# Performance work log

Hardware: AMD Instinct MI355X
Metric: run time of the kernel (lower is better)

The kernel has to match this reference:

```python
import jax, jax.numpy as jnp
import numpy as np

C = 5.0          # tanh clamp constant (args.c, non-trainable)
B, N, R, D = 4, 16, 64, 256  # batch, block_num, block_len, word_dim
NEG = -1e9


def setup_inputs() -> dict:
    key = jax.random.key(0)
    ks = iter(jax.random.split(key, 80))

    def W(i, o):
        # xavier-like init (torch stores (out,in); we store (in,out) and use x @ W)
        return jax.random.normal(next(ks), (i, o), jnp.float32) * np.float32(np.sqrt(2.0 / (i + o)))

    def bvec(d):
        return jax.random.normal(next(ks), (d,), jnp.float32) * 0.01

    inp = {"x": jax.random.normal(next(ks), (B, N, R, D), jnp.float32)}
    for p in ("fw", "bw"):
        inp[f"fcW_{p}"] = W(D, D);  inp[f"fcb_{p}"] = bvec(D)
        inp[f"mW1_{p}"] = W(D, D);  inp[f"mW2_{p}"] = W(D, D);  inp[f"mb_{p}"] = bvec(D)
        inp[f"s2tW1_{p}"] = W(D, D); inp[f"s2tb1_{p}"] = bvec(D)
        inp[f"s2tW_{p}"] = W(D, D);  inp[f"s2tb_{p}"] = bvec(D)
        inp[f"gW1_{p}"] = W(D, D);  inp[f"gW2_{p}"] = W(D, D);  inp[f"gb_{p}"] = bvec(D)
        inp[f"fW1_{p}"] = W(3 * D, D); inp[f"fb1_{p}"] = bvec(D)
        inp[f"fW2_{p}"] = W(3 * D, D); inp[f"fb2_{p}"] = bvec(D)
    return inp


def _mSA(x, W1, W2, b, fw):
    # x: (..., L, d) -> (..., L, d). Additive per-feature attention with strict
    # triangular mask. fw: token i attends to j > i (last row zeroed);
    # bw: token i attends to j < i (first row zeroed). Matches the torch
    # -inf mask + narrow + zero-pad construction exactly.
    L = x.shape[-2]
    xi = (x @ W1)[..., :, None, :]                 # (..., L, 1, d)
    xj = (x @ W2)[..., None, :, :]                 # (..., 1, L, d)
    f = C * jnp.tanh((xi + xj + b) / C)            # (..., i, j, d)
    i = jnp.arange(L)[:, None]
    j = jnp.arange(L)[None, :]
    allowed = (j > i) if fw else (j < i)           # (L, L)
    scores = jnp.where(allowed[..., None], f, NEG)
    att = jax.nn.softmax(scores, axis=-2)          # softmax over j
    rowvalid = (jnp.arange(L) < L - 1) if fw else (jnp.arange(L) > 0)
    att = att * rowvalid[:, None, None].astype(x.dtype)
    return jnp.einsum('...ijd,...jd->...id', att, x)


def _s2t(x, W1, b1, Wo, bo):
    # source2token self-attention: (..., L, d) -> (..., d)
    f = jax.nn.relu(x @ W1 + b1)
    a = jax.nn.softmax(f @ Wo + bo, axis=-2)
    return jnp.sum(a * x, axis=-2)


def _mblosa(x, mW1, mW2, mb, s2tW1, s2tb1, s2tW, s2tb,
            gW1, gW2, gb, fW1, fb1, fW2, fb2, fw):
    Bb, n, r, d = x.shape
    h = _mSA(x, mW1, mW2, mb, fw)                  # (B, n, r, d) intra-block
    v = _s2t(h, s2tW1, s2tb1, s2tW, s2tb)          # (B, n, d)    block summary
    o = _mSA(v, mW1, mW2, mb, fw)                  # (B, n, d)    inter-block
    G = jax.nn.sigmoid(o @ gW1 + v @ gW2 + gb)
    e = G * o + (1.0 - G) * v                      # (B, n, d)
    # torch: cat of e[i] repeated r times, then narrow(1, 0, n)
    idx = jnp.arange(n) // r
    E = e[:, idx]                                  # (B, n, d)
    # torch: flatten blocks then narrow(1, 0, n) (faithful to source)
    xf = x.reshape(Bb, n * r, d)[:, :n]
    hf = h.reshape(Bb, n * r, d)[:, :n]
    cat = jnp.concatenate([xf, hf, E], axis=-1)    # (B, n, 3d)
    fusion = jax.nn.relu(cat @ fW1 + fb1)
    Gf = jax.nn.sigmoid(cat @ fW2 + fb2)
    return Gf * fusion + (1.0 - Gf) * xf           # (B, n, d)


def reference(x,
              fcW_fw, fcb_fw, mW1_fw, mW2_fw, mb_fw, s2tW1_fw, s2tb1_fw,
              s2tW_fw, s2tb_fw, gW1_fw, gW2_fw, gb_fw, fW1_fw, fb1_fw,
              fW2_fw, fb2_fw,
              fcW_bw, fcb_bw, mW1_bw, mW2_bw, mb_bw, s2tW1_bw, s2tb1_bw,
              s2tW_bw, s2tb_bw, gW1_bw, gW2_bw, gb_bw, fW1_bw, fb1_bw,
              fW2_bw, fb2_bw):
    in_fw = jax.nn.relu(x @ fcW_fw + fcb_fw)
    in_bw = jax.nn.relu(x @ fcW_bw + fcb_bw)
    u_fw = _mblosa(in_fw, mW1_fw, mW2_fw, mb_fw, s2tW1_fw, s2tb1_fw,
                   s2tW_fw, s2tb_fw, gW1_fw, gW2_fw, gb_fw,
                   fW1_fw, fb1_fw, fW2_fw, fb2_fw, True)
    u_bw = _mblosa(in_bw, mW1_bw, mW2_bw, mb_bw, s2tW1_bw, s2tb1_bw,
                   s2tW_bw, s2tb_bw, gW1_bw, gW2_bw, gb_bw,
                   fW1_bw, fb1_bw, fW2_bw, fb2_bw, False)
    return jnp.concatenate([u_fw, u_bw], axis=-1)  # (B, n, 2d)
```

## Files before the change

### kernel.cpp

```cpp
#include <hip/hip_runtime.h>
#include <hip/hip_cooperative_groups.h>
#include <hip/hip_bf16.h>

typedef __hip_bfloat16 BF16;
typedef __attribute__((ext_vector_type(8))) short short8;
typedef __attribute__((ext_vector_type(4))) short short4v;
typedef __attribute__((ext_vector_type(4))) float f32x4;

#define MFMA_B16(a,b,c) __builtin_amdgcn_mfma_f32_16x16x32_bf16((a),(b),(c),0,0,0)

#if __has_builtin(__builtin_amdgcn_exp2f)
#define EXP2F(x) __builtin_amdgcn_exp2f(x)
#else
#define EXP2F(x) __expf(0.6931471805599453f * (x))
#endif

__device__ __forceinline__ short f2bs(float f){ BF16 h = __float2bfloat16(f); return *(short*)&h; }
__device__ __forceinline__ float bs2f(short s){ BF16 h = *(BF16*)&s; return __bfloat162float(h); }

struct SrcPack { const float* s[10]; };
struct GDir { const void* A0; const void* Al; const short* Wh; const short* Wl;
              const float* bias; void* O0; };
struct MbloDir { const short* Ah; const short* W1h; const short* W2h;
                 const float* mb; short* Hh; int fw; };
struct PoolDir { const short* T1; const short* Wh; const float* bias;
                 const short* Hh; float* V; };
struct Gate2Dir { const float* V; const float* W1; const float* W2; const float* mb;
                  const float* gW1; const float* gW2; const float* gb;
                  float* E0; int fw; };
struct FuseDir { const short* INh; const short* Hh;
                 const float* E0; const float* fW1; const float* fb1;
                 const float* fW2; const float* fb2; };


__global__ __launch_bounds__(256) void prep_k(SrcPack p, const float* __restrict__ X,
                                              short* __restrict__ Oh,
                                              short* __restrict__ Ol,
                                              short* __restrict__ Xh,
                                              short* __restrict__ Xl)
{
    if (blockIdx.y >= 10) {
        int u = (blockIdx.y - 10) * 16 + blockIdx.x;
        size_t base = (size_t)u * 16384;
        #pragma unroll
        for (int i = 0; i < 16; i++) {
            size_t idx = base + (size_t)i * 1024 + threadIdx.x * 4;
            float4 f = *(const float4*)(X + idx);
            short4v vh, vl;
            float t0[4] = {f.x, f.y, f.z, f.w};
            #pragma unroll
            for (int j = 0; j < 4; j++) {
                vh[j] = f2bs(t0[j]);
                vl[j] = f2bs(t0[j] - bs2f(vh[j]));
            }
            *(short4v*)(Xh + idx) = vh;
            *(short4v*)(Xl + idx) = vl;
        }
        return;
    }
    __shared__ float s[64][65];
    const float* W = p.s[blockIdx.y];
    short* oh = Oh + (size_t)blockIdx.y * 65536;
    short* ol = Ol + (size_t)blockIdx.y * 65536;
    int tr = (blockIdx.x >> 2) * 64, tc = (blockIdx.x & 3) * 64;
    #pragma unroll
    for (int i = 0; i < 16; i++) {
        int e = threadIdx.x + i * 256;
        int r = e >> 6, c = e & 63;
        s[c][r] = W[(size_t)(tr + r) * 256 + tc + c];
    }
    __syncthreads();
    #pragma unroll
    for (int i = 0; i < 16; i++) {
        int e = threadIdx.x + i * 256;
        int c2 = e >> 6, r2 = e & 63;
        float v = s[c2][r2];
        short hi = f2bs(v);
        short lo = f2bs(v - bs2f(hi));
        size_t oi = (size_t)(tc + c2) * 256 + tr + r2;
        oh[oi] = hi;
        ol[oi] = lo;
    }
}

template<int AM, int OM, int RELU, int BS>
__device__ __forceinline__ void gemm_body(const void* __restrict__ A0,
    const void* __restrict__ Alo,
    const short* __restrict__ Wh, const short* __restrict__ Wl,
    const float* __restrict__ bias, void* __restrict__ O0,
    int row0, int col0)
{
    constexpr int LDK = 72;
    __shared__ short sAh[64 * LDK];
    __shared__ short sAl[(AM == 0) ? 8 : 64 * LDK];
    __shared__ short sBh[64 * LDK];
    __shared__ short sBl[BS ? 8 : 64 * LDK];
    int tid = threadIdx.x;
    int w = tid >> 6, l = tid & 63;
    int m = l & 15, q = l >> 4;
    int sr = w * 16 + m;

    f32x4 acc[4];
    #pragma unroll
    for (int cf = 0; cf < 4; cf++) acc[cf] = (f32x4)(0.f);

    for (int kh = 0; kh < 4; kh++) {
        int kbase = kh * 64;
        #pragma unroll
        for (int i = 0; i < 2; i++) {
            int kl = q * 8 + 32 * i;
            size_t gofs = (size_t)(row0 + sr) * 256 + kbase + kl;
            if (AM == 2) {
                *(short8*)&sAh[sr * LDK + kl] = *(const short8*)((const short*)A0 + gofs);
                *(short8*)&sAl[sr * LDK + kl] = *(const short8*)((const short*)Alo + gofs);
            } else {
                *(short8*)&sAh[sr * LDK + kl] = *(const short8*)((const short*)A0 + gofs);
            }
            size_t gofsB = (size_t)(col0 + sr) * 256 + kbase + kl;
            *(short8*)&sBh[sr * LDK + kl] = *(const short8*)(Wh + gofsB);
            if (!BS)
                *(short8*)&sBl[sr * LDK + kl] = *(const short8*)(Wl + gofsB);
        }
        __syncthreads();
        #pragma unroll
        for (int ch = 0; ch < 2; ch++) {
            int k = ch * 32 + q * 8;
            short8 ah = *(const short8*)&sAh[(w * 16 + m) * LDK + k];
            short8 al = (AM != 0) ? *(const short8*)&sAl[(w * 16 + m) * LDK + k] : ah;
            #pragma unroll
            for (int cf = 0; cf < 4; cf++) {
                short8 bh = *(const short8*)&sBh[(cf * 16 + m) * LDK + k];
                acc[cf] = MFMA_B16(ah, bh, acc[cf]);
                if (!BS) {
                    short8 bl = *(const short8*)&sBl[(cf * 16 + m) * LDK + k];
                    acc[cf] = MFMA_B16(ah, bl, acc[cf]);
                }
                if (AM != 0)
                    acc[cf] = MFMA_B16(al, bh, acc[cf]);
            }
        }
        __syncthreads();
    }
    #pragma unroll
    for (int cf = 0; cf < 4; cf++) {
        int col = col0 + cf * 16 + m;
        float bv = bias ? bias[col] : 0.f;
        #pragma unroll
        for (int r = 0; r < 4; r++) {
            int row = row0 + w * 16 + q * 4 + r;
            float v = acc[cf][r] + bv;
            if (RELU) v = fmaxf(v, 0.f);
            size_t oi = (size_t)row * 256 + col;
            if (OM == 0) {
                ((float*)O0)[oi] = v;
            } else {
                ((short*)O0)[oi] = f2bs(v);
            }
        }
    }
}

template<int AM, int OM, int RELU, int BS>
__global__ __launch_bounds__(256) void gemm_k(GDir p0, GDir p1)
{
    GDir p = blockIdx.z ? p1 : p0;
    gemm_body<AM, OM, RELU, BS>(p.A0, p.Al, p.Wh, p.Wl, p.bias, p.O0,
                                blockIdx.x * 64, blockIdx.y * 64);
}

__global__ __launch_bounds__(512) void mblo_k(MbloDir p0, MbloDir p1)
{
    __shared__ char smraw[33536] __attribute__((aligned(16)));
    short* gAh  = (short*)smraw;
    short* gB1h = gAh + 4608;
    short* gB2h = gAh + 9216;
    float* aP   = (float*)smraw;
    unsigned int* aQX = (unsigned int*)(smraw + 16896);

    const float KLN = -0.06931471805599453f;

    MbloDir p = blockIdx.z ? p1 : p0;
    int tid = threadIdx.x;
    int w = tid >> 6, l = tid & 63;
    int m = l & 15, q = l >> 4;
    int rh = w >> 1;
    int cb = (w & 1) * 2;
    int bn = blockIdx.x >> 1, ipar = blockIdx.x & 1;
    int row0 = bn * 64, d0 = blockIdx.y * 64;
    int srow = tid >> 3;
    int skl  = (tid & 7) * 8;

    f32x4 acc1[2], acc2[2];
    #pragma unroll
    for (int cf = 0; cf < 2; cf++) { acc1[cf] = (f32x4)(0.f); acc2[cf] = (f32x4)(0.f); }

    for (int kh = 0; kh < 4; kh++) {
        int kbase = kh * 64;
        size_t ga = (size_t)(row0 + srow) * 256 + kbase + skl;
        *(short8*)&gAh[srow * 72 + skl] = *(const short8*)(p.Ah + ga);
        size_t gb = (size_t)(d0 + srow) * 256 + kbase + skl;
        *(short8*)&gB1h[srow * 72 + skl] = *(const short8*)(p.W1h + gb);
        *(short8*)&gB2h[srow * 72 + skl] = *(const short8*)(p.W2h + gb);
        __syncthreads();
        #pragma unroll
        for (int ch = 0; ch < 2; ch++) {
            int k = ch * 32 + q * 8;
            short8 ah = *(const short8*)&gAh[(rh * 16 + m) * 72 + k];
            #pragma unroll
            for (int cf = 0; cf < 2; cf++) {
                int bofs = ((cb + cf) * 16 + m) * 72 + k;
                short8 b1 = *(const short8*)&gB1h[bofs];
                acc1[cf] = MFMA_B16(ah, b1, acc1[cf]);
                short8 b2 = *(const short8*)&gB2h[bofs];
                acc2[cf] = MFMA_B16(ah, b2, acc2[cf]);
            }
        }
        __syncthreads();
    }
    short* sQX = (short*)aQX;
    #pragma unroll
    for (int cf = 0; cf < 2; cf++) {
        int col = (cb + cf) * 16 + m;
        float mbv = p.mb[d0 + col];
        #pragma unroll
        for (int r = 0; r < 4; r++) {
            int row = rh * 16 + q * 4 + r;
            aP[row * 66 + col] = __expf(0.4f * acc1[cf][r]) * KLN;
            sQX[col * 130 + 2 * row] = f2bs(__expf(0.4f * (acc2[cf][r] + mbv)));
        }
    }
    {
        size_t gx = (size_t)(row0 + srow) * 256 + d0 + skl;
        short8 xh = *(const short8*)(p.Ah + gx);
        #pragma unroll
        for (int t = 0; t < 8; t++)
            sQX[(skl + t) * 130 + 2 * srow + 1] = xh[t];
    }
    __syncthreads();
    const unsigned int* lane_qx = &aQX[l * 65];
    #pragma unroll
    for (int t8 = 0; t8 < 4; t8++) {
        int i = ipar + 2 * (w + 8 * t8);
        float Pp = aP[i * 66 + l];
        int js = p.fw ? (i + 1) : 0;
        int je = p.fw ? 64 : i;
        float den0 = 0.f, den1 = 0.f, num0 = 0.f, num1 = 0.f;
        int j = js;
        for (; j + 4 <= je; j += 4) {
            unsigned int u0 = lane_qx[j];
            unsigned int u1 = lane_qx[j + 1];
            unsigned int u2 = lane_qx[j + 2];
            unsigned int u3 = lane_qx[j + 3];
            float q0 = bs2f((short)(u0 & 0xffff)), x0 = bs2f((short)(u0 >> 16));
            float q1 = bs2f((short)(u1 & 0xffff)), x1 = bs2f((short)(u1 >> 16));
            float q2 = bs2f((short)(u2 & 0xffff)), x2 = bs2f((short)(u2 >> 16));
            float q3 = bs2f((short)(u3 & 0xffff)), x3 = bs2f((short)(u3 >> 16));
            float w0 = EXP2F(__builtin_amdgcn_rcpf(fmaf(Pp, q0, KLN)));
            float w1 = EXP2F(__builtin_amdgcn_rcpf(fmaf(Pp, q1, KLN)));
            float w2 = EXP2F(__builtin_amdgcn_rcpf(fmaf(Pp, q2, KLN)));
            float w3 = EXP2F(__builtin_amdgcn_rcpf(fmaf(Pp, q3, KLN)));
            den0 += w0; num0 = fmaf(w0, x0, num0);
            den1 += w1; num1 = fmaf(w1, x1, num1);
            den0 += w2; num0 = fmaf(w2, x2, num0);
            den1 += w3; num1 = fmaf(w3, x3, num1);
        }
        for (; j < je; j++) {
            unsigned int u0 = lane_qx[j];
            float q0 = bs2f((short)(u0 & 0xffff)), x0 = bs2f((short)(u0 >> 16));
            float wgt = EXP2F(__builtin_amdgcn_rcpf(fmaf(Pp, q0, KLN)));
            den0 += wgt; num0 = fmaf(wgt, x0, num0);
        }
        float den = den0 + den1, num = num0 + num1;
        bool valid = p.fw ? (i < 63) : (i > 0);
        float out = valid ? (num * __builtin_amdgcn_rcpf(den)) : 0.f;
        p.Hh[(size_t)(row0 + i) * 256 + d0 + l] = f2bs(out);
    }
}

__global__ __launch_bounds__(256) void s2t_pool_k(PoolDir p0, PoolDir p1)
{
    __shared__ char smraw[37888] __attribute__((aligned(16)));
    short* gAh = (short*)smraw;
    short* gBh = gAh + 4608;
    float* aL = (float*)smraw;
    float* aH = aL + 4352;
    float* rm = aL + 8704;
    float* rd = aL + 8960;
    float* rn = aL + 9216;

    PoolDir p = blockIdx.z ? p1 : p0;
    int tid = threadIdx.x;
    int w = tid >> 6, l = tid & 63;
    int m = l & 15, q = l >> 4;
    int sr = w * 16 + m;
    int row0 = blockIdx.x * 64, d0 = blockIdx.y * 64;

    f32x4 acc[4];
    #pragma unroll
    for (int cf = 0; cf < 4; cf++) acc[cf] = (f32x4)(0.f);

    for (int kh = 0; kh < 4; kh++) {
        int kbase = kh * 64;
        #pragma unroll
        for (int i = 0; i < 2; i++) {
            int kl = q * 8 + 32 * i;
            *(short8*)&gAh[sr * 72 + kl] =
                *(const short8*)(p.T1 + (size_t)(row0 + sr) * 256 + kbase + kl);
            *(short8*)&gBh[sr * 72 + kl] =
                *(const short8*)(p.Wh + (size_t)(d0 + sr) * 256 + kbase + kl);
        }
        __syncthreads();
        #pragma unroll
        for (int ch = 0; ch < 2; ch++) {
            int k = ch * 32 + q * 8;
            short8 ah = *(const short8*)&gAh[(w * 16 + m) * 72 + k];
            #pragma unroll
            for (int cf = 0; cf < 4; cf++) {
                short8 bh = *(const short8*)&gBh[(cf * 16 + m) * 72 + k];
                acc[cf] = MFMA_B16(ah, bh, acc[cf]);
            }
        }
        __syncthreads();
    }
    #pragma unroll
    for (int cf = 0; cf < 4; cf++) {
        int col = cf * 16 + m;
        float bv = p.bias[d0 + col];
        #pragma unroll
        for (int r = 0; r < 4; r++) {
            int row = w * 16 + q * 4 + r;
            aL[row * 68 + col] = acc[cf][r] + bv;
        }
    }
    #pragma unroll
    for (int it = 0; it < 2; it++) {
        int e = tid + it * 256;
        int j = e >> 3, d8 = (e & 7) * 8;
        short8 xh = *(const short8*)(p.Hh + (size_t)(row0 + j) * 256 + d0 + d8);
        #pragma unroll
        for (int t = 0; t < 8; t++)
            aH[j * 68 + d8 + t] = bs2f(xh[t]);
    }
    __syncthreads();
    int dl = tid & 63, rq = tid >> 6;
    float mx = -1e30f, den = 0.f, num = 0.f;
    #pragma unroll
    for (int rr = 0; rr < 16; rr++) {
        int r = rq * 16 + rr;
        float lv = aL[r * 68 + dl];
        float hv = aH[r * 68 + dl];
        if (lv > mx) {
            float sc = __expf(mx - lv);
            den *= sc; num *= sc; mx = lv;
        }
        float wgt = __expf(lv - mx);
        den += wgt; num += wgt * hv;
    }
    rm[rq * 64 + dl] = mx; rd[rq * 64 + dl] = den; rn[rq * 64 + dl] = num;
    __syncthreads();
    if (rq == 0) {
        float M = fmaxf(fmaxf(rm[dl], rm[64 + dl]), fmaxf(rm[128 + dl], rm[192 + dl]));
        float D = 0.f, Nn = 0.f;
        #pragma unroll
        for (int k = 0; k < 4; k++) {
            float sc = __expf(rm[k * 64 + dl] - M);
            D += rd[k * 64 + dl] * sc;
            Nn += rn[k * 64 + dl] * sc;
        }
        p.V[(size_t)blockIdx.x * 256 + d0 + dl] = Nn / D;
    }
}

__global__ __launch_bounds__(512) void attn2gate_k(Gate2Dir p0, Gate2Dir p1)
{
    Gate2Dir p = blockIdx.z ? p1 : p0;
    __shared__ __attribute__((aligned(16))) float sVT[4096];
    __shared__ float sPart[16][256];
    __shared__ float so[256], sv[256], red[8][64];
    int tid = threadIdx.x;
    int b = blockIdx.x;
    int k = tid & 255, half = tid >> 8;

    if (p.fw) {
        #pragma unroll
        for (int it = 0; it < 8; it++) {
            int e = tid + it * 512;
            int kk = e >> 4, j = e & 15;
            sVT[e] = p.V[(size_t)(b * 16 + j) * 256 + kk];
        }
        __syncthreads();
        float acc[16];
        #pragma unroll
        for (int j = 0; j < 16; j++) acc[j] = 0.f;
        int kk0 = half * 128;
        #pragma unroll 4
        for (int kk = kk0; kk < kk0 + 128; kk++) {
            const float4* vr = (const float4*)&sVT[kk * 16];
            float4 va = vr[0], vb = vr[1], vc = vr[2], vd = vr[3];
            float w1 = p.W1[(size_t)kk * 256 + k];
            float w2 = p.W2[(size_t)kk * 256 + k];
            acc[0]  = fmaf(va.x, w1, acc[0]);
            acc[1]  = fmaf(va.y, w2, acc[1]);
            acc[2]  = fmaf(va.z, w2, acc[2]);
            acc[3]  = fmaf(va.w, w2, acc[3]);
            acc[4]  = fmaf(vb.x, w2, acc[4]);
            acc[5]  = fmaf(vb.y, w2, acc[5]);
            acc[6]  = fmaf(vb.z, w2, acc[6]);
            acc[7]  = fmaf(vb.w, w2, acc[7]);
            acc[8]  = fmaf(vc.x, w2, acc[8]);
            acc[9]  = fmaf(vc.y, w2, acc[9]);
            acc[10] = fmaf(vc.z, w2, acc[10]);
            acc[11] = fmaf(vc.w, w2, acc[11]);
            acc[12] = fmaf(vd.x, w2, acc[12]);
            acc[13] = fmaf(vd.y, w2, acc[13]);
            acc[14] = fmaf(vd.z, w2, acc[14]);
            acc[15] = fmaf(vd.w, w2, acc[15]);
        }
        if (half) {
            #pragma unroll
            for (int j = 0; j < 16; j++) sPart[j][k] = acc[j];
        }
        __syncthreads();
        if (!half) {
            #pragma unroll
            for (int j = 0; j < 16; j++) acc[j] += sPart[j][k];
            float base = acc[0] + p.mb[k];
            float den = 0.f, num = 0.f;
            #pragma unroll
            for (int j = 1; j < 16; j++) {
                float z = (base + acc[j]) * 0.2f;
                float e2 = __expf(2.f * z);
                float t = 1.f - 2.f / (e2 + 1.f);
                float wgt = __expf(5.f * t);
                den += wgt;
                num = fmaf(wgt, p.V[(size_t)(b * 16 + j) * 256 + k], num);
            }
            so[k] = num / den;
            sv[k] = p.V[(size_t)(b * 16) * 256 + k];
        }
    } else {
        if (!half) {
            so[k] = 0.f;
            sv[k] = p.V[(size_t)(b * 16) * 256 + k];
        }
    }
    __syncthreads();
    int c = tid & 63, ks = tid >> 6;
    int gc = blockIdx.y * 64 + c;
    float a2 = 0.f;
    int k0 = ks * 32;
    #pragma unroll 8
    for (int kkx = 0; kkx < 32; kkx++) {
        int kx = k0 + kkx;
        a2 += so[kx] * p.gW1[(size_t)kx * 256 + gc] + sv[kx] * p.gW2[(size_t)kx * 256 + gc];
    }
    red[ks][c] = a2;
    __syncthreads();
    if (ks == 0) {
        float a = red[0][c] + red[1][c] + red[2][c] + red[3][c]
                + red[4][c] + red[5][c] + red[6][c] + red[7][c] + p.gb[gc];
        float G = 1.f / (1.f + __expf(-a));
        p.E0[b * 256 + gc] = G * so[gc] + (1.f - G) * sv[gc];
    }
}

__global__ __launch_bounds__(256) void fusion_k(FuseDir p0, FuseDir p1, float* __restrict__ out)
{
    FuseDir p = blockIdx.z ? p1 : p0;
    __shared__ float cat[768];
    __shared__ float red1[4][64], red2[4][64];
    int bt = blockIdx.x, b = bt >> 4, t = bt & 15;
    int c = threadIdx.x & 63, ks = threadIdx.x >> 6;
    int gc = blockIdx.y * 64 + c;
    size_t xrow = ((size_t)b * 1024 + t) * 256;
    cat[threadIdx.x]       = bs2f(p.INh[xrow + threadIdx.x]);
    cat[256 + threadIdx.x] = bs2f(p.Hh[xrow + threadIdx.x]);
    cat[512 + threadIdx.x] = p.E0[b * 256 + threadIdx.x];
    __syncthreads();
    float a1 = 0.f, a2 = 0.f;
    int k0 = ks * 192;
    #pragma unroll 8
    for (int kk = 0; kk < 192; kk++) {
        int k = k0 + kk;
        float cv = cat[k];
        a1 += cv * p.fW1[(size_t)k * 256 + gc];
        a2 += cv * p.fW2[(size_t)k * 256 + gc];
    }
    red1[ks][c] = a1; red2[ks][c] = a2;
    __syncthreads();
    if (ks == 0) {
        float s1 = red1[0][c] + red1[1][c] + red1[2][c] + red1[3][c] + p.fb1[gc];
        float s2 = red2[0][c] + red2[1][c] + red2[2][c] + red2[3][c] + p.fb2[gc];
        float fus = fmaxf(s1, 0.f);
        float Gf = 1.f / (1.f + __expf(-s2));
        float u = Gf * fus + (1.f - Gf) * cat[gc];
        out[((size_t)(b * 16 + t)) * 512 + (size_t)blockIdx.z * 256 + gc] = u;
    }
}


struct MegaP {
    SrcPack sp; const float* X;
    short *wtH, *wtL, *xh, *xl;
    GDir fc[2], s2t1[2];
    MbloDir mbd[2];
    PoolDir pld[2];
    Gate2Dir gtd[2];
    FuseDir fsd[2];
    float* out;
};

template<int AM, int OM, int RELU, int BS>
__device__ __forceinline__ void gemm512(const void* __restrict__ A0,
    const void* __restrict__ Alo,
    const short* __restrict__ Wh, const short* __restrict__ Wl,
    const float* __restrict__ bias, void* __restrict__ O0,
    int row0, int col0, char* SM)
{
    short* sAh = (short*)SM;
    short* sAl = (short*)(SM + 9216);
    short* sBh = (short*)(SM + 18432);
    short* sBl = (short*)(SM + 27648);
    int tid = threadIdx.x;
    int w = tid >> 6, l = tid & 63, m = l & 15, q = l >> 4;
    int strip = w >> 1, chalf = w & 1;
    int srow = tid >> 3, skl = (tid & 7) * 8;
    f32x4 acc[2];
    acc[0] = (f32x4)(0.f); acc[1] = (f32x4)(0.f);
    for (int kh = 0; kh < 4; kh++) {
        int kb = kh * 64;
        size_t ga = (size_t)(row0 + srow) * 256 + kb + skl;
        *(short8*)&sAh[srow * 72 + skl] = *(const short8*)((const short*)A0 + ga);
        if (AM == 2)
            *(short8*)&sAl[srow * 72 + skl] = *(const short8*)((const short*)Alo + ga);
        size_t gb = (size_t)(col0 + srow) * 256 + kb + skl;
        *(short8*)&sBh[srow * 72 + skl] = *(const short8*)(Wh + gb);
        if (!BS)
            *(short8*)&sBl[srow * 72 + skl] = *(const short8*)(Wl + gb);
        __syncthreads();
        #pragma unroll
        for (int ch = 0; ch < 2; ch++) {
            int k = ch * 32 + q * 8;
            short8 ah = *(const short8*)&sAh[(strip * 16 + m) * 72 + k];
            short8 al = (AM == 2) ? *(const short8*)&sAl[(strip * 16 + m) * 72 + k] : ah;
            #pragma unroll
            for (int cf = 0; cf < 2; cf++) {
                int bofs = ((chalf * 2 + cf) * 16 + m) * 72 + k;
                short8 bh = *(const short8*)&sBh[bofs];
                acc[cf] = MFMA_B16(ah, bh, acc[cf]);
                if (!BS) {
                    short8 bl = *(const short8*)&sBl[bofs];
                    acc[cf] = MFMA_B16(ah, bl, acc[cf]);
                }
                if (AM == 2)
                    acc[cf] = MFMA_B16(al, bh, acc[cf]);
            }
        }
        __syncthreads();
    }
    #pragma unroll
    for (int cf = 0; cf < 2; cf++) {
        int col = col0 + (chalf * 2 + cf) * 16 + m;
        float bv = bias ? bias[col] : 0.f;
        #pragma unroll
        for (int r = 0; r < 4; r++) {
            int row = row0 + strip * 16 + q * 4 + r;
            float v = acc[cf][r] + bv;
            if (RELU) v = fmaxf(v, 0.f);
            size_t oi = (size_t)row * 256 + col;
            if (OM == 0) ((float*)O0)[oi] = v;
            else ((short*)O0)[oi] = f2bs(v);
        }
    }
}

__global__ __launch_bounds__(512) void mega_k(MegaP mp)
{
    __shared__ char SM[40960] __attribute__((aligned(16)));
    cooperative_groups::grid_group gg = cooperative_groups::this_grid();
    const int tid = threadIdx.x;
    const int bid = blockIdx.x, nb = gridDim.x;
    const float KLN = -0.06931471805599453f;

    for (int job = bid; job < 224; job += nb) {
        if (job < 160) {
            int mat = job >> 4, tile = job & 15;
            float (*s)[65] = (float(*)[65])SM;
            const float* W = mp.sp.s[mat];
            short* oh = mp.wtH + (size_t)mat * 65536;
            short* ol = mp.wtL + (size_t)mat * 65536;
            int tr = (tile >> 2) * 64, tc = (tile & 3) * 64;
            #pragma unroll
            for (int i = 0; i < 8; i++) {
                int e = tid + i * 512;
                int r = e >> 6, c = e & 63;
                s[c][r] = W[(size_t)(tr + r) * 256 + tc + c];
            }
            __syncthreads();
            #pragma unroll
            for (int i = 0; i < 8; i++) {
                int e = tid + i * 512;
                int c2 = e >> 6, r2 = e & 63;
                float v = s[c2][r2];
                short hi = f2bs(v);
                short lo = f2bs(v - bs2f(hi));
                size_t oi = (size_t)(tc + c2) * 256 + tr + r2;
                oh[oi] = hi;
                ol[oi] = lo;
            }
            __syncthreads();
        } else {
            int u = job - 160;
            size_t base = (size_t)u * 16384;
            #pragma unroll
            for (int i = 0; i < 8; i++) {
                size_t idx = base + (size_t)i * 2048 + tid * 4;
                float4 f = *(const float4*)(mp.X + idx);
                short4v vh, vl;
                float t0[4] = {f.x, f.y, f.z, f.w};
                #pragma unroll
                for (int j = 0; j < 4; j++) {
                    vh[j] = f2bs(t0[j]);
                    vl[j] = f2bs(t0[j] - bs2f(vh[j]));
                }
                *(short4v*)(mp.xh + idx) = vh;
                *(short4v*)(mp.xl + idx) = vl;
            }
        }
    }
    gg.sync();

    for (int job = bid; job < 512; job += nb) {
        int dir = job >> 8, rem = job & 255;
        GDir p = mp.fc[dir];
        gemm512<2, 1, 1, 0>(p.A0, p.Al, p.Wh, p.Wl, p.bias, p.O0,
                            (rem & 63) * 64, (rem >> 6) * 64, SM);
    }
    gg.sync();

    {
        short* gAh  = (short*)SM;
        short* gB1h = gAh + 4608;
        short* gB2h = gAh + 9216;
        float* aP   = (float*)SM;
        unsigned int* aQX = (unsigned int*)(SM + 16896);
        int w = tid >> 6, l = tid & 63, m = l & 15, q = l >> 4;
        int rh = w >> 1, cb = (w & 1) * 2;
        int srow = tid >> 3, skl = (tid & 7) * 8;
        for (int job = bid; job < 512; job += nb) {
            int dir = job >> 8, rem = job & 255;
            MbloDir p = mp.mbd[dir];
            int row0 = (rem & 63) * 64, d0 = (rem >> 6) * 64;
            f32x4 acc1[2], acc2[2];
            #pragma unroll
            for (int cf = 0; cf < 2; cf++) { acc1[cf] = (f32x4)(0.f); acc2[cf] = (f32x4)(0.f); }
            for (int kh = 0; kh < 4; kh++) {
                int kbase = kh * 64;
                size_t ga = (size_t)(row0 + srow) * 256 + kbase + skl;
                *(short8*)&gAh[srow * 72 + skl] = *(const short8*)(p.Ah + ga);
                size_t gb = (size_t)(d0 + srow) * 256 + kbase + skl;
                *(short8*)&gB1h[srow * 72 + skl] = *(const short8*)(p.W1h + gb);
                *(short8*)&gB2h[srow * 72 + skl] = *(const short8*)(p.W2h + gb);
                __syncthreads();
                #pragma unroll
                for (int ch = 0; ch < 2; ch++) {
                    int k = ch * 32 + q * 8;
                    short8 ah = *(const short8*)&gAh[(rh * 16 + m) * 72 + k];
                    #pragma unroll
                    for (int cf = 0; cf < 2; cf++) {
                        int bofs = ((cb + cf) * 16 + m) * 72 + k;
                        short8 b1 = *(const short8*)&gB1h[bofs];
                        acc1[cf] = MFMA_B16(ah, b1, acc1[cf]);
                        short8 b2 = *(const short8*)&gB2h[bofs];
                        acc2[cf] = MFMA_B16(ah, b2, acc2[cf]);
                    }
                }
                __syncthreads();
            }
            short* sQX = (short*)aQX;
            #pragma unroll
            for (int cf = 0; cf < 2; cf++) {
                int col = (cb + cf) * 16 + m;
                float mbv = p.mb[d0 + col];
                #pragma unroll
                for (int r = 0; r < 4; r++) {
                    int row = rh * 16 + q * 4 + r;
                    aP[row * 66 + col] = __expf(0.4f * acc1[cf][r]) * KLN;
                    sQX[col * 130 + 2 * row] = f2bs(__expf(0.4f * (acc2[cf][r] + mbv)));
                }
            }
            {
                size_t gx = (size_t)(row0 + srow) * 256 + d0 + skl;
                short8 xh = *(const short8*)(p.Ah + gx);
                #pragma unroll
                for (int t = 0; t < 8; t++)
                    sQX[(skl + t) * 130 + 2 * srow + 1] = xh[t];
            }
            __syncthreads();
            const unsigned int* lane_qx = &aQX[l * 65];
            for (int t8 = 0; t8 < 8; t8++) {
                int i = w + 8 * t8;
                float Pp = aP[i * 66 + l];
                int js = p.fw ? (i + 1) : 0;
                int je = p.fw ? 64 : i;
                float den0 = 0.f, den1 = 0.f, num0 = 0.f, num1 = 0.f;
                int j = js;
                for (; j + 4 <= je; j += 4) {
                    unsigned int u0 = lane_qx[j];
                    unsigned int u1 = lane_qx[j + 1];
                    unsigned int u2 = lane_qx[j + 2];
                    unsigned int u3 = lane_qx[j + 3];
                    float q0 = bs2f((short)(u0 & 0xffff)), x0 = bs2f((short)(u0 >> 16));
                    float q1 = bs2f((short)(u1 & 0xffff)), x1 = bs2f((short)(u1 >> 16));
                    float q2 = bs2f((short)(u2 & 0xffff)), x2 = bs2f((short)(u2 >> 16));
                    float q3 = bs2f((short)(u3 & 0xffff)), x3 = bs2f((short)(u3 >> 16));
                    float w0 = EXP2F(__builtin_amdgcn_rcpf(fmaf(Pp, q0, KLN)));
                    float w1 = EXP2F(__builtin_amdgcn_rcpf(fmaf(Pp, q1, KLN)));
                    float w2 = EXP2F(__builtin_amdgcn_rcpf(fmaf(Pp, q2, KLN)));
                    float w3 = EXP2F(__builtin_amdgcn_rcpf(fmaf(Pp, q3, KLN)));
                    den0 += w0; num0 = fmaf(w0, x0, num0);
                    den1 += w1; num1 = fmaf(w1, x1, num1);
                    den0 += w2; num0 = fmaf(w2, x2, num0);
                    den1 += w3; num1 = fmaf(w3, x3, num1);
                }
                for (; j < je; j++) {
                    unsigned int u0 = lane_qx[j];
                    float q0 = bs2f((short)(u0 & 0xffff)), x0 = bs2f((short)(u0 >> 16));
                    float wgt = EXP2F(__builtin_amdgcn_rcpf(fmaf(Pp, q0, KLN)));
                    den0 += wgt; num0 = fmaf(wgt, x0, num0);
                }
                float den = den0 + den1, num = num0 + num1;
                bool valid = p.fw ? (i < 63) : (i > 0);
                float out = valid ? (num * __builtin_amdgcn_rcpf(den)) : 0.f;
                p.Hh[(size_t)(row0 + i) * 256 + d0 + l] = f2bs(out);
            }
            __syncthreads();
        }
    }
    gg.sync();

    for (int job = bid; job < 512; job += nb) {
        int dir = job >> 8, rem = job & 255;
        GDir p = mp.s2t1[dir];
        gemm512<0, 1, 1, 1>(p.A0, nullptr, p.Wh, nullptr, p.bias, p.O0,
                            (rem & 63) * 64, (rem >> 6) * 64, SM);
    }
    gg.sync();

    {
        short* gAh = (short*)SM;
        short* gBh = gAh + 4608;
        float* aL = (float*)SM;
        float* aH = aL + 4352;
        float* rm = (float*)(SM + 34816);
        float* rd = rm + 512;
        float* rn = rm + 1024;
        int w = tid >> 6, l = tid & 63, m = l & 15, q = l >> 4;
        int strip = w >> 1, chalf = w & 1;
        int srow = tid >> 3, skl = (tid & 7) * 8;
        for (int job = bid; job < 512; job += nb) {
            int dir = job >> 8, rem = job & 255;
            PoolDir p = mp.pld[dir];
            int row0 = (rem & 63) * 64, d0 = (rem >> 6) * 64;
            f32x4 acc[2];
            acc[0] = (f32x4)(0.f); acc[1] = (f32x4)(0.f);
            for (int kh = 0; kh < 4; kh++) {
                int kbase = kh * 64;
                *(short8*)&gAh[srow * 72 + skl] =
                    *(const short8*)(p.T1 + (size_t)(row0 + srow) * 256 + kbase + skl);
                *(short8*)&gBh[srow * 72 + skl] =
                    *(const short8*)(p.Wh + (size_t)(d0 + srow) * 256 + kbase + skl);
                __syncthreads();
                #pragma unroll
                for (int ch = 0; ch < 2; ch++) {
                    int k = ch * 32 + q * 8;
                    short8 ah = *(const short8*)&gAh[(strip * 16 + m) * 72 + k];
                    #pragma unroll
                    for (int cf = 0; cf < 2; cf++) {
                        short8 bh = *(const short8*)&gBh[((chalf * 2 + cf) * 16 + m) * 72 + k];
                        acc[cf] = MFMA_B16(ah, bh, acc[cf]);
                    }
                }
                __syncthreads();
            }
            #pragma unroll
            for (int cf = 0; cf < 2; cf++) {
                int col = (chalf * 2 + cf) * 16 + m;
                float bv = p.bias[d0 + col];
                #pragma unroll
                for (int r = 0; r < 4; r++) {
                    int row = strip * 16 + q * 4 + r;
                    aL[row * 68 + col] = acc[cf][r] + bv;
                }
            }
            {
                int j = tid >> 3, d8 = (tid & 7) * 8;
                short8 xh = *(const short8*)(p.Hh + (size_t)(row0 + j) * 256 + d0 + d8);
                #pragma unroll
                for (int t = 0; t < 8; t++)
                    aH[j * 68 + d8 + t] = bs2f(xh[t]);
            }
            __syncthreads();
            int dl = tid & 63, rq = tid >> 6;
            float mx = -1e30f, den = 0.f, num = 0.f;
            #pragma unroll
            for (int rr = 0; rr < 8; rr++) {
                int r = rq * 8 + rr;
                float lv = aL[r * 68 + dl];
                float hv = aH[r * 68 + dl];
                if (lv > mx) { float sc = __expf(mx - lv); den *= sc; num *= sc; mx = lv; }
                float wgt = __expf(lv - mx);
                den += wgt; num = fmaf(wgt, hv, num);
            }
            rm[rq * 64 + dl] = mx; rd[rq * 64 + dl] = den; rn[rq * 64 + dl] = num;
            __syncthreads();
            if (rq == 0) {
                float M = rm[dl];
                #pragma unroll
                for (int kq = 1; kq < 8; kq++) M = fmaxf(M, rm[kq * 64 + dl]);
                float D = 0.f, Nn = 0.f;
                #pragma unroll
                for (int kq = 0; kq < 8; kq++) {
                    float sc = __expf(rm[kq * 64 + dl] - M);
                    D += rd[kq * 64 + dl] * sc;
                    Nn += rn[kq * 64 + dl] * sc;
                }
                p.V[(size_t)(rem & 63) * 256 + d0 + dl] = Nn / D;
            }
            __syncthreads();
        }
    }
    gg.sync();

    {
        float* sVT = (float*)SM;
        float (*sPart)[256] = (float(*)[256])(SM + 16384);
        float* so = (float*)(SM + 32768);
        float* sv = (float*)(SM + 33792);
        float (*red)[64] = (float(*)[64])(SM + 34816);
        for (int job = bid; job < 32; job += nb) {
            int b = job & 3, gy = (job >> 2) & 3, dir = job >> 4;
            Gate2Dir p = mp.gtd[dir];
            int k = tid & 255, half = tid >> 8;
            if (p.fw) {
                #pragma unroll
                for (int it = 0; it < 8; it++) {
                    int e = tid + it * 512;
                    int kk = e >> 4, j = e & 15;
                    sVT[e] = p.V[(size_t)(b * 16 + j) * 256 + kk];
                }
                __syncthreads();
                float acc[16];
                #pragma unroll
                for (int j = 0; j < 16; j++) acc[j] = 0.f;
                int kk0 = half * 128;
                #pragma unroll 4
                for (int kk = kk0; kk < kk0 + 128; kk++) {
                    const float4* vr = (const float4*)&sVT[kk * 16];
                    float4 va = vr[0], vb = vr[1], vc = vr[2], vd = vr[3];
                    float w1 = p.W1[(size_t)kk * 256 + k];
                    float w2 = p.W2[(size_t)kk * 256 + k];
                    acc[0]  = fmaf(va.x, w1, acc[0]);
                    acc[1]  = fmaf(va.y, w2, acc[1]);
                    acc[2]  = fmaf(va.z, w2, acc[2]);
                    acc[3]  = fmaf(va.w, w2, acc[3]);
                    acc[4]  = fmaf(vb.x, w2, acc[4]);
                    acc[5]  = fmaf(vb.y, w2, acc[5]);
                    acc[6]  = fmaf(vb.z, w2, acc[6]);
                    acc[7]  = fmaf(vb.w, w2, acc[7]);
                    acc[8]  = fmaf(vc.x, w2, acc[8]);
                    acc[9]  = fmaf(vc.y, w2, acc[9]);
                    acc[10] = fmaf(vc.z, w2, acc[10]);
                    acc[11] = fmaf(vc.w, w2, acc[11]);
                    acc[12] = fmaf(vd.x, w2, acc[12]);
                    acc[13] = fmaf(vd.y, w2, acc[13]);
                    acc[14] = fmaf(vd.z, w2, acc[14]);
                    acc[15] = fmaf(vd.w, w2, acc[15]);
                }
                if (half) {
                    #pragma unroll
                    for (int j = 0; j < 16; j++) sPart[j][k] = acc[j];
                }
                __syncthreads();
                if (!half) {
                    #pragma unroll
                    for (int j = 0; j < 16; j++) acc[j] += sPart[j][k];
                    float base = acc[0] + p.mb[k];
                    float den = 0.f, num = 0.f;
                    #pragma unroll
                    for (int j = 1; j < 16; j++) {
                        float z = (base + acc[j]) * 0.2f;
                        float e2 = __expf(2.f * z);
                        float t = 1.f - 2.f / (e2 + 1.f);
                        float wgt = __expf(5.f * t);
                        den += wgt;
                        num = fmaf(wgt, p.V[(size_t)(b * 16 + j) * 256 + k], num);
                    }
                    so[k] = num / den;
                    sv[k] = p.V[(size_t)(b * 16) * 256 + k];
                }
            } else {
                if (!half) {
                    so[k] = 0.f;
                    sv[k] = p.V[(size_t)(b * 16) * 256 + k];
                }
            }
            __syncthreads();
            int c = tid & 63, ks = tid >> 6;
            int gc = gy * 64 + c;
            float a2 = 0.f;
            int k0 = ks * 32;
            #pragma unroll 8
            for (int kkx = 0; kkx < 32; kkx++) {
                int kx = k0 + kkx;
                a2 += so[kx] * p.gW1[(size_t)kx * 256 + gc] + sv[kx] * p.gW2[(size_t)kx * 256 + gc];
            }
            red[ks][c] = a2;
            __syncthreads();
            if (ks == 0) {
                float a = red[0][c] + red[1][c] + red[2][c] + red[3][c]
                        + red[4][c] + red[5][c] + red[6][c] + red[7][c] + p.gb[gc];
                float G = 1.f / (1.f + __expf(-a));
                p.E0[b * 256 + gc] = G * so[gc] + (1.f - G) * sv[gc];
            }
            __syncthreads();
        }
    }
    gg.sync();

    {
        float* cat = (float*)SM;
        float (*red1)[64] = (float(*)[64])(SM + 3072);
        float (*red2)[64] = (float(*)[64])(SM + 5120);
        for (int job = bid; job < 512; job += nb) {
            int dir = job >> 8, rem = job & 255;
            int bt = rem & 63, gy = rem >> 6;
            FuseDir p = mp.fsd[dir];
            int b = bt >> 4, t = bt & 15;
            size_t xrow = ((size_t)b * 1024 + t) * 256;
            if (tid < 256) {
                cat[tid] = bs2f(p.INh[xrow + tid]);
                cat[512 + tid] = p.E0[b * 256 + tid];
            } else {
                cat[tid] = bs2f(p.Hh[xrow + tid - 256]);
            }
            __syncthreads();
            int c = tid & 63, ks = tid >> 6;
            int gc = gy * 64 + c;
            float a1 = 0.f, a2 = 0.f;
            int k0 = ks * 96;
            #pragma unroll 8
            for (int kk = 0; kk < 96; kk++) {
                int k = k0 + kk;
                float cv = cat[k];
                a1 += cv * p.fW1[(size_t)k * 256 + gc];
                a2 += cv * p.fW2[(size_t)k * 256 + gc];
            }
            red1[ks][c] = a1; red2[ks][c] = a2;
            __syncthreads();
            if (ks == 0) {
                float s1 = p.fb1[gc], s2 = p.fb2[gc];
                #pragma unroll
                for (int kq = 0; kq < 8; kq++) { s1 += red1[kq][c]; s2 += red2[kq][c]; }
                float fus = fmaxf(s1, 0.f);
                float Gf = 1.f / (1.f + __expf(-s2));
                float u = Gf * fus + (1.f - Gf) * cat[gc];
                mp.out[((size_t)(b * 16 + t)) * 512 + (size_t)dir * 256 + gc] = u;
            }
            __syncthreads();
        }
    }
}


extern "C" void kernel_launch(void* const* d_in, const int* in_sizes, int n_in,
                              void* d_out, int out_size, void* d_ws, size_t ws_size,
                              hipStream_t stream)
{
    const float* x = (const float*)d_in[0];
    char* base = (char*)d_ws;
    auto alloc = [&](size_t bytes){ void* r = base; base += (bytes + 255) & ~255ULL; return r; };
    short* inH = (short*)alloc(2 * 1048576 * 2);
    short* hH  = (short*)alloc(2 * 1048576 * 2);
    short* t1  = (short*)alloc(2 * 1048576 * 2);
    short* wtH = (short*)alloc(10 * 65536 * 2);
    short* wtL = (short*)alloc(10 * 65536 * 2);
    short* xh  = (short*)alloc(1048576 * 2);
    short* xl  = (short*)alloc(1048576 * 2);
    float* v   = (float*)alloc(2 * 16384 * 4);
    float* E0  = (float*)alloc(2 * 1024 * 4);

    SrcPack sp;
    const int src_idx[5] = {0, 2, 3, 5, 7};
    for (int p = 0; p < 2; p++)
        for (int i = 0; i < 5; i++)
            sp.s[p * 5 + i] = (const float*)d_in[1 + p * 16 + src_idx[i]];

    GDir fc[2], s2t1[2];
    MbloDir mbd[2];
    PoolDir pld[2];
    Gate2Dir gtd[2];
    FuseDir fsd[2];
    for (int p = 0; p < 2; p++) {
        int bi = 1 + p * 16;
        const float* fcb   = (const float*)d_in[bi + 1];
        const float* mb    = (const float*)d_in[bi + 4];
        const float* s2tb1 = (const float*)d_in[bi + 6];
        const float* s2tb  = (const float*)d_in[bi + 8];
        size_t po = (size_t)p * 1048576;
        const short* W0h = wtH + (size_t)(p * 5 + 0) * 65536, *W0l = wtL + (size_t)(p * 5 + 0) * 65536;
        const short* W1h = wtH + (size_t)(p * 5 + 1) * 65536;
        const short* W2h = wtH + (size_t)(p * 5 + 2) * 65536;
        const short* W3h = wtH + (size_t)(p * 5 + 3) * 65536;
        const short* W4h = wtH + (size_t)(p * 5 + 4) * 65536;

        fc[p]   = { xh, xl, W0h, W0l, fcb, inH + po };
        mbd[p]  = { inH + po, W1h, W2h, mb, hH + po, (p == 0) };
        s2t1[p] = { hH + po, nullptr, W3h, nullptr, s2tb1, t1 + po };
        pld[p]  = { t1 + po, W4h, s2tb, hH + po, v + p * 16384 };
        gtd[p]  = { v + p * 16384,
                    (const float*)d_in[bi + 2], (const float*)d_in[bi + 3], mb,
                    (const float*)d_in[bi + 9], (const float*)d_in[bi + 10],
                    (const float*)d_in[bi + 11], E0 + p * 1024, (p == 0) };
        fsd[p]  = { inH + po, hH + po, E0 + p * 1024,
                    (const float*)d_in[bi + 12], (const float*)d_in[bi + 13],
                    (const float*)d_in[bi + 14], (const float*)d_in[bi + 15] };
    }

    static int coopGrid = -2;
    if (coopGrid == -2) {
        int perCU = 0;
        hipError_t e1 = hipOccupancyMaxActiveBlocksPerMultiprocessor(&perCU, mega_k, 512, 0);
        if (e1 == hipSuccess && perCU > 0) {
            hipDeviceProp_t prop;
            int dev = 0;
            hipGetDevice(&dev);
            if (hipGetDeviceProperties(&prop, dev) == hipSuccess && prop.cooperativeLaunch) {
                long g = (long)perCU * prop.multiProcessorCount;
                coopGrid = (int)(g > 512 ? 512 : g);
            } else coopGrid = -1;
        } else coopGrid = -1;
    }

    bool done = false;
    if (coopGrid > 0) {
        MegaP mp;
        mp.sp = sp; mp.X = x;
        mp.wtH = wtH; mp.wtL = wtL; mp.xh = xh; mp.xl = xl;
        for (int p = 0; p < 2; p++) {
            mp.fc[p] = fc[p]; mp.s2t1[p] = s2t1[p];
            mp.mbd[p] = mbd[p]; mp.pld[p] = pld[p];
            mp.gtd[p] = gtd[p]; mp.fsd[p] = fsd[p];
        }
        mp.out = (float*)d_out;
        void* kargs[] = { (void*)&mp };
        if (hipLaunchCooperativeKernel((void*)mega_k, dim3(coopGrid), dim3(512),
                                       kargs, 0, stream) == hipSuccess)
            done = true;
        else
            coopGrid = -1;
    }

    if (!done) {
        prep_k<<<dim3(16, 14), 256, 0, stream>>>(sp, x, wtH, wtL, xh, xl);
        gemm_k<2, 1, 1, 0><<<dim3(64, 4, 2), 256, 0, stream>>>(fc[0], fc[1]);
        mblo_k<<<dim3(128, 4, 2), 512, 0, stream>>>(mbd[0], mbd[1]);
        gemm_k<0, 1, 1, 1><<<dim3(64, 4, 2), 256, 0, stream>>>(s2t1[0], s2t1[1]);
        s2t_pool_k<<<dim3(64, 4, 2), 256, 0, stream>>>(pld[0], pld[1]);
        attn2gate_k<<<dim3(4, 4, 2), 512, 0, stream>>>(gtd[0], gtd[1]);
        fusion_k<<<dim3(64, 4, 2), 256, 0, stream>>>(fsd[0], fsd[1], (float*)d_out);
    }
}
```

Measured before the change: 209.8 us.

## Replace cooperative grid sync with atomic barriers and fuse prep into FC GEMM

Swaps the cooperative launch and grid.sync for a normal launch of a persistent kernel that synchronises through hand-written atomic counter barriers, which are zeroed with a memset before each launch. Converting x and the FC weight to hi/lo bf16 now happens inside the FC GEMM's tile loads rather than in a separate prep pass. The remaining weights are converted to hi only, and the xh/xl/wtL scratch buffers are dropped. On the fallback path, the s2t GEMM and pooling are merged into one kernel. Spin barriers without a cooperative launch can deadlock if not every block is resident, and the converted W0 is re-read from fp32 by every tile.

```diff
diff --git a/kernel.cpp b/kernel.cpp
--- a/kernel.cpp
+++ b/kernel.cpp
@@ -1,10 +1,8 @@
 #include <hip/hip_runtime.h>
-#include <hip/hip_cooperative_groups.h>
 #include <hip/hip_bf16.h>
 
 typedef __hip_bfloat16 BF16;
 typedef __attribute__((ext_vector_type(8))) short short8;
-typedef __attribute__((ext_vector_type(4))) short short4v;
 typedef __attribute__((ext_vector_type(4))) float f32x4;
 
 #define MFMA_B16(a,b,c) __builtin_amdgcn_mfma_f32_16x16x32_bf16((a),(b),(c),0,0,0)
@@ -18,11 +16,18 @@
 __device__ __forceinline__ short f2bs(float f){ BF16 h = __float2bfloat16(f); return *(short*)&h; }
 __device__ __forceinline__ float bs2f(short s){ BF16 h = *(BF16*)&s; return __bfloat162float(h); }
 
-struct SrcPack { const float* s[10]; };
+struct FcPrepP {
+    const float* X;
+    const float* W0[2];
+    const float* fcb[2];
+    short* inH[2];
+    const float* wsrc[8];
+    short* wdst[8];
+};
+struct MbloDir { const short* Ah; const short* W1h; const short* W2h;
+                 const float* mb; short* Hh; int fw; };
 struct GDir { const void* A0; const void* Al; const short* Wh; const short* Wl;
               const float* bias; void* O0; };
-struct MbloDir { const short* Ah; const short* W1h; const short* W2h;
-                 const float* mb; short* Hh; int fw; };
 struct PoolDir { const short* T1; const short* Wh; const float* bias;
                  const short* Hh; float* V; };
 struct Gate2Dir { const float* V; const float* W1; const float* W2; const float* mb;
@@ -33,72 +38,49 @@
                  const float* fW2; const float* fb2; };
 
 
-__global__ __launch_bounds__(256) void prep_k(SrcPack p, const float* __restrict__ X,
-                                              short* __restrict__ Oh,
-                                              short* __restrict__ Ol,
-                                              short* __restrict__ Xh,
-                                              short* __restrict__ Xl)
+__global__ __launch_bounds__(256) void fcprep_k(FcPrepP P)
 {
-    if (blockIdx.y >= 10) {
-        int u = (blockIdx.y - 10) * 16 + blockIdx.x;
-        size_t base = (size_t)u * 16384;
+    __shared__ char SM[36864] __attribute__((aligned(16)));
+    int job = blockIdx.x;
+    int tid = threadIdx.x;
+
+    if (job >= 512) {
+        int mi = job - 512;
+        int mat = mi >> 4, tile = mi & 15;
+        float (*s)[65] = (float(*)[65])SM;
+        const float* W = P.wsrc[mat];
+        short* oh = P.wdst[mat];
+        int tr = (tile >> 2) * 64, tc = (tile & 3) * 64;
         #pragma unroll
         for (int i = 0; i < 16; i++) {
-            size_t idx = base + (size_t)i * 1024 + threadIdx.x * 4;
-            float4 f = *(const float4*)(X + idx);
-            short4v vh, vl;
-            float t0[4] = {f.x, f.y, f.z, f.w};
-            #pragma unroll
-            for (int j = 0; j < 4; j++) {
-                vh[j] = f2bs(t0[j]);
-                vl[j] = f2bs(t0[j] - bs2f(vh[j]));
-            }
-            *(short4v*)(Xh + idx) = vh;
-            *(short4v*)(Xl + idx) = vl;
+            int e = tid + i * 256;
+            int r = e >> 6, c = e & 63;
+            s[c][r] = W[(size_t)(tr + r) * 256 + tc + c];
+        }
+        __syncthreads();
+        #pragma unroll
+        for (int i = 0; i < 16; i++) {
+            int e = tid + i * 256;
+            int c2 = e >> 6, r2 = e & 63;
+            oh[(size_t)(tc + c2) * 256 + tr + r2] = f2bs(s[c2][r2]);
         }
         return;
     }
-    __shared__ float s[64][65];
-    const float* W = p.s[blockIdx.y];
-    short* oh = Oh + (size_t)blockIdx.y * 65536;
-    short* ol = Ol + (size_t)blockIdx.y * 65536;
-    int tr = (blockIdx.x >> 2) * 64, tc = (blockIdx.x & 3) * 64;
-    #pragma unroll
-    for (int i = 0; i < 16; i++) {
-        int e = threadIdx.x + i * 256;
-        int r = e >> 6, c = e & 63;
-        s[c][r] = W[(size_t)(tr + r) * 256 + tc + c];
-    }
-    __syncthreads();
-    #pragma unroll
-    for (int i = 0; i < 16; i++) {
-        int e = threadIdx.x + i * 256;
-        int c2 = e >> 6, r2 = e & 63;
-        float v = s[c2][r2];
-        short hi = f2bs(v);
-        short lo = f2bs(v - bs2f(hi));
-        size_t oi = (size_t)(tc + c2) * 256 + tr + r2;
-        oh[oi] = hi;
-        ol[oi] = lo;
-    }
-}
-
-template<int AM, int OM, int RELU, int BS>
-__device__ __forceinline__ void gemm_body(const void* __restrict__ A0,
-    const void* __restrict__ Alo,
-    const short* __restrict__ Wh, const short* __restrict__ Wl,
-    const float* __restrict__ bias, void* __restrict__ O0,
-    int row0, int col0)
-{
-    constexpr int LDK = 72;
-    __shared__ short sAh[64 * LDK];
-    __shared__ short sAl[(AM == 0) ? 8 : 64 * LDK];
-    __shared__ short sBh[64 * LDK];
-    __shared__ short sBl[BS ? 8 : 64 * LDK];
-    int tid = threadIdx.x;
+
+    short* sAh = (short*)SM;
+    short* sAl = sAh + 4608;
+    short* sBh = sAh + 9216;
+    short* sBl = sAh + 13824;
+    int dir = job >> 8, rem = job & 255;
+    int row0 = (rem & 63) * 64, col0 = (rem >> 6) * 64;
+    const float* W0 = P.W0[dir];
+    const float* bias = P.fcb[dir];
+    short* O = P.inH[dir];
+
     int w = tid >> 6, l = tid & 63;
     int m = l & 15, q = l >> 4;
     int sr = w * 16 + m;
+    int bcc = tid >> 2, bkk0 = (tid & 3) * 16;
 
     f32x4 acc[4];
     #pragma unroll
@@ -110,33 +92,50 @@
         for (int i = 0; i < 2; i++) {
             int kl = q * 8 + 32 * i;
             size_t gofs = (size_t)(row0 + sr) * 256 + kbase + kl;
-            if (AM == 2) {
-                *(short8*)&sAh[sr * LDK + kl] = *(const short8*)((const short*)A0 + gofs);
-                *(short8*)&sAl[sr * LDK + kl] = *(const short8*)((const short*)Alo + gofs);
-            } else {
-                *(short8*)&sAh[sr * LDK + kl] = *(const short8*)((const short*)A0 + gofs);
-            }
-            size_t gofsB = (size_t)(col0 + sr) * 256 + kbase + kl;
-            *(short8*)&sBh[sr * LDK + kl] = *(const short8*)(Wh + gofsB);
-            if (!BS)
-                *(short8*)&sBl[sr * LDK + kl] = *(const short8*)(Wl + gofsB);
+            const float* src = P.X + gofs;
+            float4 f0 = *(const float4*)src;
+            float4 f1 = *(const float4*)(src + 4);
+            short8 vh, vl;
+            float tmp[8] = {f0.x, f0.y, f0.z, f0.w, f1.x, f1.y, f1.z, f1.w};
+            #pragma unroll
+            for (int j = 0; j < 8; j++) {
+                vh[j] = f2bs(tmp[j]);
+                vl[j] = f2bs(tmp[j] - bs2f(vh[j]));
+            }
+            *(short8*)&sAh[sr * 72 + kl] = vh;
+            *(short8*)&sAl[sr * 72 + kl] = vl;
+        }
+        {
+            float vals[16];
+            #pragma unroll
+            for (int j = 0; j < 16; j++)
+                vals[j] = W0[(size_t)(kbase + bkk0 + j) * 256 + col0 + bcc];
+            #pragma unroll
+            for (int h8 = 0; h8 < 2; h8++) {
+                short8 vh, vl;
+                #pragma unroll
+                for (int j = 0; j < 8; j++) {
+                    float v = vals[h8 * 8 + j];
+                    vh[j] = f2bs(v);
+                    vl[j] = f2bs(v - bs2f(vh[j]));
+                }
+                *(short8*)&sBh[bcc * 72 + bkk0 + h8 * 8] = vh;
+                *(short8*)&sBl[bcc * 72 + bkk0 + h8 * 8] = vl;
+            }
         }
         __syncthreads();
         #pragma unroll
         for (int ch = 0; ch < 2; ch++) {
             int k = ch * 32 + q * 8;
-            short8 ah = *(const short8*)&sAh[(w * 16 + m) * LDK + k];
-            short8 al = (AM != 0) ? *(const short8*)&sAl[(w * 16 + m) * LDK + k] : ah;
+            short8 ah = *(const short8*)&sAh[(w * 16 + m) * 72 + k];
+            short8 al = *(const short8*)&sAl[(w * 16 + m) * 72 + k];
             #pragma unroll
             for (int cf = 0; cf < 4; cf++) {
-                short8 bh = *(const short8*)&sBh[(cf * 16 + m) * LDK + k];
+                short8 bh = *(const short8*)&sBh[(cf * 16 + m) * 72 + k];
                 acc[cf] = MFMA_B16(ah, bh, acc[cf]);
-                if (!BS) {
-                    short8 bl = *(const short8*)&sBl[(cf * 16 + m) * LDK + k];
-                    acc[cf] = MFMA_B16(ah, bl, acc[cf]);
-                }
-                if (AM != 0)
-                    acc[cf] = MFMA_B16(al, bh, acc[cf]);
+                short8 bl = *(const short8*)&sBl[(cf * 16 + m) * 72 + k];
+                acc[cf] = MFMA_B16(ah, bl, acc[cf]);
+                acc[cf] = MFMA_B16(al, bh, acc[cf]);
             }
         }
         __syncthreads();
@@ -144,28 +143,14 @@
     #pragma unroll
     for (int cf = 0; cf < 4; cf++) {
         int col = col0 + cf * 16 + m;
-        float bv = bias ? bias[col] : 0.f;
+        float bv = bias[col];
         #pragma unroll
         for (int r = 0; r < 4; r++) {
             int row = row0 + w * 16 + q * 4 + r;
-            float v = acc[cf][r] + bv;
-            if (RELU) v = fmaxf(v, 0.f);
-            size_t oi = (size_t)row * 256 + col;
-            if (OM == 0) {
-                ((float*)O0)[oi] = v;
-            } else {
-                ((short*)O0)[oi] = f2bs(v);
-            }
-        }
-    }
-}
-
-template<int AM, int OM, int RELU, int BS>
-__global__ __launch_bounds__(256) void gemm_k(GDir p0, GDir p1)
-{
-    GDir p = blockIdx.z ? p1 : p0;
-    gemm_body<AM, OM, RELU, BS>(p.A0, p.Al, p.Wh, p.Wl, p.bias, p.O0,
-                                blockIdx.x * 64, blockIdx.y * 64);
+            float v = fmaxf(acc[cf][r] + bv, 0.f);
+            O[(size_t)row * 256 + col] = f2bs(v);
+        }
+    }
 }
 
 __global__ __launch_bounds__(512) void mblo_k(MbloDir p0, MbloDir p1)
@@ -277,95 +262,122 @@
     }
 }
 
-__global__ __launch_bounds__(256) void s2t_pool_k(PoolDir p0, PoolDir p1)
+struct S2TDir { const short* Hh; const short* W3h; const float* b1;
+                const short* W4h; const float* b2; float* V; };
+
+__global__ __launch_bounds__(512) void s2t_fused_k(S2TDir p0, S2TDir p1)
 {
-    __shared__ char smraw[37888] __attribute__((aligned(16)));
-    short* gAh = (short*)smraw;
-    short* gBh = gAh + 4608;
-    float* aL = (float*)smraw;
-    float* aH = aL + 4352;
-    float* rm = aL + 8704;
-    float* rd = aL + 8960;
-    float* rn = aL + 9216;
-
-    PoolDir p = blockIdx.z ? p1 : p0;
+    __shared__ char smraw[79872] __attribute__((aligned(16)));
+    short* sT1 = (short*)smraw;
+    short* gA  = (short*)(smraw + 33792);
+    short* gB  = (short*)(smraw + 43008);
+    short* gB2 = (short*)(smraw + 33792);
+    float* aL  = (float*)(smraw + 43008);
+    float* rm  = (float*)(smraw + 60416);
+    float* rd  = rm + 512;
+    float* rn  = rm + 1024;
+
+    S2TDir p = blockIdx.z ? p1 : p0;
     int tid = threadIdx.x;
     int w = tid >> 6, l = tid & 63;
     int m = l & 15, q = l >> 4;
-    int sr = w * 16 + m;
-    int row0 = blockIdx.x * 64, d0 = blockIdx.y * 64;
-
-    f32x4 acc[4];
+    int row0 = blockIdx.x * 64;
+    int d0 = blockIdx.y * 64;
+    int strip = w >> 1, chalf = w & 1;
+    int srow = tid >> 3, skl = (tid & 7) * 8;
+
+    f32x4 acc1[8];
     #pragma unroll
-    for (int cf = 0; cf < 4; cf++) acc[cf] = (f32x4)(0.f);
-
+    for (int cf = 0; cf < 8; cf++) acc1[cf] = (f32x4)(0.f);
     for (int kh = 0; kh < 4; kh++) {
         int kbase = kh * 64;
-        #pragma unroll
-        for (int i = 0; i < 2; i++) {
-            int kl = q * 8 + 32 * i;
-            *(short8*)&gAh[sr * 72 + kl] =
-                *(const short8*)(p.T1 + (size_t)(row0 + sr) * 256 + kbase + kl);
-            *(short8*)&gBh[sr * 72 + kl] =
-                *(const short8*)(p.Wh + (size_t)(d0 + sr) * 256 + kbase + kl);
+        *(short8*)&gA[srow * 72 + skl] =
+            *(const short8*)(p.Hh + (size_t)(row0 + srow) * 256 + kbase + skl);
+        int bn = tid >> 1;
+        #pragma unroll
+        for (int i = 0; i < 4; i++) {
+            int kseg = (tid & 1) * 32 + i * 8;
+            *(short8*)&gB[bn * 72 + kseg] =
+                *(const short8*)(p.W3h + (size_t)bn * 256 + kbase + kseg);
         }
         __syncthreads();
         #pragma unroll
         for (int ch = 0; ch < 2; ch++) {
             int k = ch * 32 + q * 8;
-            short8 ah = *(const short8*)&gAh[(w * 16 + m) * 72 + k];
-            #pragma unroll
-            for (int cf = 0; cf < 4; cf++) {
-                short8 bh = *(const short8*)&gBh[(cf * 16 + m) * 72 + k];
-                acc[cf] = MFMA_B16(ah, bh, acc[cf]);
+            short8 ah = *(const short8*)&gA[(strip * 16 + m) * 72 + k];
+            #pragma unroll
+            for (int cf = 0; cf < 8; cf++) {
+                short8 bh = *(const short8*)&gB[(chalf * 128 + cf * 16 + m) * 72 + k];
+                acc1[cf] = MFMA_B16(ah, bh, acc1[cf]);
             }
         }
         __syncthreads();
     }
     #pragma unroll
-    for (int cf = 0; cf < 4; cf++) {
-        int col = cf * 16 + m;
-        float bv = p.bias[d0 + col];
+    for (int cf = 0; cf < 8; cf++) {
+        int col = chalf * 128 + cf * 16 + m;
+        float bv = p.b1[col];
         #pragma unroll
         for (int r = 0; r < 4; r++) {
-            int row = w * 16 + q * 4 + r;
-            aL[row * 68 + col] = acc[cf][r] + bv;
-        }
+            int row = strip * 16 + q * 4 + r;
+            sT1[row * 264 + col] = f2bs(fmaxf(acc1[cf][r] + bv, 0.f));
+        }
+    }
+    __syncthreads();
+
+    f32x4 acc2[2];
+    acc2[0] = (f32x4)(0.f); acc2[1] = (f32x4)(0.f);
+    for (int kh = 0; kh < 4; kh++) {
+        int kbase = kh * 64;
+        *(short8*)&gB2[srow * 72 + skl] =
+            *(const short8*)(p.W4h + (size_t)(d0 + srow) * 256 + kbase + skl);
+        __syncthreads();
+        #pragma unroll
+        for (int ch = 0; ch < 2; ch++) {
+            int k = ch * 32 + q * 8;
+            short8 ah = *(const short8*)&sT1[(strip * 16 + m) * 264 + kbase + k];
+            #pragma unroll
+            for (int cf = 0; cf < 2; cf++) {
+                short8 bh = *(const short8*)&gB2[(chalf * 32 + cf * 16 + m) * 72 + k];
+                acc2[cf] = MFMA_B16(ah, bh, acc2[cf]);
+            }
+        }
+        __syncthreads();
     }
     #pragma unroll
-    for (int it = 0; it < 2; it++) {
-        int e = tid + it * 256;
-        int j = e >> 3, d8 = (e & 7) * 8;
-        short8 xh = *(const short8*)(p.Hh + (size_t)(row0 + j) * 256 + d0 + d8);
-        #pragma unroll
-        for (int t = 0; t < 8; t++)
-            aH[j * 68 + d8 + t] = bs2f(xh[t]);
+    for (int cf = 0; cf < 2; cf++) {
+        int col = chalf * 32 + cf * 16 + m;
+        float bv = p.b2[d0 + col];
+        #pragma unroll
+        for (int r = 0; r < 4; r++) {
+            int row = strip * 16 + q * 4 + r;
+            aL[row * 68 + col] = acc2[cf][r] + bv;
+        }
     }
     __syncthreads();
     int dl = tid & 63, rq = tid >> 6;
     float mx = -1e30f, den = 0.f, num = 0.f;
     #pragma unroll
-    for (int rr = 0; rr < 16; rr++) {
-        int r = rq * 16 + rr;
+    for (int rr = 0; rr < 8; rr++) {
+        int r = rq * 8 + rr;
         float lv = aL[r * 68 + dl];
-        float hv = aH[r * 68 + dl];
-        if (lv > mx) {
-            float sc = __expf(mx - lv);
-            den *= sc; num *= sc; mx = lv;
-        }
+        float hv = bs2f(p.Hh[(size_t)(row0 + r) * 256 + d0 + dl]);
+        if (lv > mx) { float sc = __expf(mx - lv); den *= sc; num *= sc; mx = lv; }
         float wgt = __expf(lv - mx);
-        den += wgt; num += wgt * hv;
+        den += wgt; num = fmaf(wgt, hv, num);
     }
     rm[rq * 64 + dl] = mx; rd[rq * 64 + dl] = den; rn[rq * 64 + dl] = num;
     __syncthreads();
     if (rq == 0) {
-        float M = fmaxf(fmaxf(rm[dl], rm[64 + dl]), fmaxf(rm[128 + dl], rm[192 + dl]));
+        float M = rm[dl];
+        #pragma unroll
+        for (int kq = 1; kq < 8; kq++) M = fmaxf(M, rm[kq * 64 + dl]);
         float D = 0.f, Nn = 0.f;
         #pragma unroll
-        for (int k = 0; k < 4; k++) {
-            float sc = __expf(rm[k * 64 + dl] - M);
-            D += rd[k * 64 + dl] * sc;
-            Nn += rn[k * 64 + dl] * sc;
+        for (int kq = 0; kq < 8; kq++) {
+            float sc = __expf(rm[kq * 64 + dl] - M);
+            D += rd[kq * 64 + dl] * sc;
+            Nn += rn[kq * 64 + dl] * sc;
         }
         p.V[(size_t)blockIdx.x * 256 + d0 + dl] = Nn / D;
     }
@@ -499,28 +511,44 @@
 }
 
 
-struct MegaP {
-    SrcPack sp; const float* X;
-    short *wtH, *wtL, *xh, *xl;
-    GDir fc[2], s2t1[2];
+struct PersP {
+    const float* X;
+    const float* W0[2]; const float* fcb[2]; short* inH[2];
+    const float* wsrc[8]; short* wdst[8];
     MbloDir mbd[2];
+    GDir s2t1[2];
     PoolDir pld[2];
     Gate2Dir gtd[2];
     FuseDir fsd[2];
     float* out;
+    unsigned* bars;
 };
 
-template<int AM, int OM, int RELU, int BS>
-__device__ __forceinline__ void gemm512(const void* __restrict__ A0,
-    const void* __restrict__ Alo,
-    const short* __restrict__ Wh, const short* __restrict__ Wl,
-    const float* __restrict__ bias, void* __restrict__ O0,
-    int row0, int col0, char* SM)
+__device__ __forceinline__ void gbar(unsigned* bar, int nb)
+{
+    __syncthreads();
+    if (threadIdx.x == 0) {
+        __threadfence();
+        unsigned arrived = __hip_atomic_fetch_add(bar, 1u, __ATOMIC_ACQ_REL,
+                                                  __HIP_MEMORY_SCOPE_AGENT) + 1u;
+        if (arrived == (unsigned)nb) {
+            __hip_atomic_store(bar + 1, 1u, __ATOMIC_RELEASE, __HIP_MEMORY_SCOPE_AGENT);
+        } else {
+            while (__hip_atomic_load(bar + 1, __ATOMIC_ACQUIRE,
+                                     __HIP_MEMORY_SCOPE_AGENT) == 0u)
+                __builtin_amdgcn_s_sleep(2);
+        }
+        __threadfence();
+    }
+    __syncthreads();
+}
+
+__device__ __forceinline__ void gemm512_s(const short* __restrict__ A0,
+    const short* __restrict__ Wh, const float* __restrict__ bias,
+    short* __restrict__ O0, int row0, int col0, char* SM)
 {
     short* sAh = (short*)SM;
-    short* sAl = (short*)(SM + 9216);
     short* sBh = (short*)(SM + 18432);
-    short* sBl = (short*)(SM + 27648);
     int tid = threadIdx.x;
     int w = tid >> 6, l = tid & 63, m = l & 15, q = l >> 4;
     int strip = w >> 1, chalf = w & 1;
@@ -530,30 +558,18 @@
     for (int kh = 0; kh < 4; kh++) {
         int kb = kh * 64;
         size_t ga = (size_t)(row0 + srow) * 256 + kb + skl;
-        *(short8*)&sAh[srow * 72 + skl] = *(const short8*)((const short*)A0 + ga);
-        if (AM == 2)
-            *(short8*)&sAl[srow * 72 + skl] = *(const short8*)((const short*)Alo + ga);
+        *(short8*)&sAh[srow * 72 + skl] = *(const short8*)(A0 + ga);
         size_t gb = (size_t)(col0 + srow) * 256 + kb + skl;
         *(short8*)&sBh[srow * 72 + skl] = *(const short8*)(Wh + gb);
-        if (!BS)
-            *(short8*)&sBl[srow * 72 + skl] = *(const short8*)(Wl + gb);
         __syncthreads();
         #pragma unroll
         for (int ch = 0; ch < 2; ch++) {
             int k = ch * 32 + q * 8;
             short8 ah = *(const short8*)&sAh[(strip * 16 + m) * 72 + k];
-            short8 al = (AM == 2) ? *(const short8*)&sAl[(strip * 16 + m) * 72 + k] : ah;
             #pragma unroll
             for (int cf = 0; cf < 2; cf++) {
-                int bofs = ((chalf * 2 + cf) * 16 + m) * 72 + k;
-                short8 bh = *(const short8*)&sBh[bofs];
+                short8 bh = *(const short8*)&sBh[((chalf * 2 + cf) * 16 + m) * 72 + k];
                 acc[cf] = MFMA_B16(ah, bh, acc[cf]);
-                if (!BS) {
-                    short8 bl = *(const short8*)&sBl[bofs];
-                    acc[cf] = MFMA_B16(ah, bl, acc[cf]);
-                }
-                if (AM == 2)
-                    acc[cf] = MFMA_B16(al, bh, acc[cf]);
             }
         }
         __syncthreads();
@@ -561,34 +577,29 @@
     #pragma unroll
     for (int cf = 0; cf < 2; cf++) {
         int col = col0 + (chalf * 2 + cf) * 16 + m;
-        float bv = bias ? bias[col] : 0.f;
+        float bv = bias[col];
         #pragma unroll
         for (int r = 0; r < 4; r++) {
             int row = row0 + strip * 16 + q * 4 + r;
-            float v = acc[cf][r] + bv;
-            if (RELU) v = fmaxf(v, 0.f);
-            size_t oi = (size_t)row * 256 + col;
-            if (OM == 0) ((float*)O0)[oi] = v;
-            else ((short*)O0)[oi] = f2bs(v);
+            O0[(size_t)row * 256 + col] = f2bs(fmaxf(acc[cf][r] + bv, 0.f));
         }
     }
 }
 
-__global__ __launch_bounds__(512) void mega_k(MegaP mp)
+__global__ __launch_bounds__(512) void pers_k(PersP P)
 {
     __shared__ char SM[40960] __attribute__((aligned(16)));
-    cooperative_groups::grid_group gg = cooperative_groups::this_grid();
     const int tid = threadIdx.x;
     const int bid = blockIdx.x, nb = gridDim.x;
     const float KLN = -0.06931471805599453f;
 
-    for (int job = bid; job < 224; job += nb) {
-        if (job < 160) {
-            int mat = job >> 4, tile = job & 15;
+    for (int job = bid; job < 640; job += nb) {
+        if (job >= 512) {
+            int mi = job - 512;
+            int mat = mi >> 4, tile = mi & 15;
             float (*s)[65] = (float(*)[65])SM;
-            const float* W = mp.sp.s[mat];
-            short* oh = mp.wtH + (size_t)mat * 65536;
-            short* ol = mp.wtL + (size_t)mat * 65536;
+            const float* W = P.wsrc[mat];
+            short* oh = P.wdst[mat];
             int tr = (tile >> 2) * 64, tc = (tile & 3) * 64;
             #pragma unroll
             for (int i = 0; i < 8; i++) {
@@ -601,42 +612,87 @@
             for (int i = 0; i < 8; i++) {
                 int e = tid + i * 512;
                 int c2 = e >> 6, r2 = e & 63;
-                float v = s[c2][r2];
-                short hi = f2bs(v);
-                short lo = f2bs(v - bs2f(hi));
-                size_t oi = (size_t)(tc + c2) * 256 + tr + r2;
-                oh[oi] = hi;
-                ol[oi] = lo;
-            }
-            __syncthreads();
-        } else {
-            int u = job - 160;
-            size_t base = (size_t)u * 16384;
-            #pragma unroll
-            for (int i = 0; i < 8; i++) {
-                size_t idx = base + (size_t)i * 2048 + tid * 4;
-                float4 f = *(const float4*)(mp.X + idx);
-                short4v vh, vl;
-                float t0[4] = {f.x, f.y, f.z, f.w};
-                #pragma unroll
-                for (int j = 0; j < 4; j++) {
-                    vh[j] = f2bs(t0[j]);
-                    vl[j] = f2bs(t0[j] - bs2f(vh[j]));
-                }
-                *(short4v*)(mp.xh + idx) = vh;
-                *(short4v*)(mp.xl + idx) = vl;
-            }
-        }
-    }
-    gg.sync();
-
-    for (int job = bid; job < 512; job += nb) {
+                oh[(size_t)(tc + c2) * 256 + tr + r2] = f2bs(s[c2][r2]);
+            }
+            __syncthreads();
+            continue;
+        }
+        short* sAh = (short*)SM;
+        short* sAl = sAh + 4608;
+        short* sBh = sAh + 9216;
+        short* sBl = sAh + 13824;
         int dir = job >> 8, rem = job & 255;
-        GDir p = mp.fc[dir];
-        gemm512<2, 1, 1, 0>(p.A0, p.Al, p.Wh, p.Wl, p.bias, p.O0,
-                            (rem & 63) * 64, (rem >> 6) * 64, SM);
-    }
-    gg.sync();
+        int row0 = (rem & 63) * 64, col0 = (rem >> 6) * 64;
+        const float* W0 = P.W0[dir];
+        const float* bias = P.fcb[dir];
+        short* O = P.inH[dir];
+        int w = tid >> 6, l = tid & 63, m = l & 15, q = l >> 4;
+        int strip = w >> 1, chalf = w & 1;
+        int srow = tid >> 3, skl = (tid & 7) * 8;
+        int bcc = tid >> 3, bkk0 = (tid & 7) * 8;
+        f32x4 acc[2];
+        acc[0] = (f32x4)(0.f); acc[1] = (f32x4)(0.f);
+        for (int kh = 0; kh < 4; kh++) {
+            int kbase = kh * 64;
+            {
+                size_t gofs = (size_t)(row0 + srow) * 256 + kbase + skl;
+                const float* src = P.X + gofs;
+                float4 f0 = *(const float4*)src;
+                float4 f1 = *(const float4*)(src + 4);
+                short8 vh, vl;
+                float tmp[8] = {f0.x, f0.y, f0.z, f0.w, f1.x, f1.y, f1.z, f1.w};
+                #pragma unroll
+                for (int j = 0; j < 8; j++) {
+                    vh[j] = f2bs(tmp[j]);
+                    vl[j] = f2bs(tmp[j] - bs2f(vh[j]));
+                }
+                *(short8*)&sAh[srow * 72 + skl] = vh;
+                *(short8*)&sAl[srow * 72 + skl] = vl;
+            }
+            {
+                float vals[8];
+                #pragma unroll
+                for (int j = 0; j < 8; j++)
+                    vals[j] = W0[(size_t)(kbase + bkk0 + j) * 256 + col0 + bcc];
+                short8 vh, vl;
+                #pragma unroll
+                for (int j = 0; j < 8; j++) {
+                    vh[j] = f2bs(vals[j]);
+                    vl[j] = f2bs(vals[j] - bs2f(vh[j]));
+                }
+                *(short8*)&sBh[bcc * 72 + bkk0] = vh;
+                *(short8*)&sBl[bcc * 72 + bkk0] = vl;
+            }
+            __syncthreads();
+            #pragma unroll
+            for (int ch = 0; ch < 2; ch++) {
+                int k = ch * 32 + q * 8;
+                short8 ah = *(const short8*)&sAh[(strip * 16 + m) * 72 + k];
+                short8 al = *(const short8*)&sAl[(strip * 16 + m) * 72 + k];
+                #pragma unroll
+                for (int cf = 0; cf < 2; cf++) {
+                    int bofs = ((chalf * 2 + cf) * 16 + m) * 72 + k;
+                    short8 bh = *(const short8*)&sBh[bofs];
+                    acc[cf] = MFMA_B16(ah, bh, acc[cf]);
+                    short8 bl = *(const short8*)&sBl[bofs];
+                    acc[cf] = MFMA_B16(ah, bl, acc[cf]);
+                    acc[cf] = MFMA_B16(al, bh, acc[cf]);
+                }
+            }
+            __syncthreads();
+        }
+        #pragma unroll
+        for (int cf = 0; cf < 2; cf++) {
+            int col = col0 + (chalf * 2 + cf) * 16 + m;
+            float bv = bias[col];
+            #pragma unroll
+            for (int r = 0; r < 4; r++) {
+                int row = row0 + strip * 16 + q * 4 + r;
+                O[(size_t)row * 256 + col] = f2bs(fmaxf(acc[cf][r] + bv, 0.f));
+            }
+        }
+    }
+    gbar(P.bars + 0, nb);
 
     {
         short* gAh  = (short*)SM;
@@ -649,7 +705,7 @@
         int srow = tid >> 3, skl = (tid & 7) * 8;
         for (int job = bid; job < 512; job += nb) {
             int dir = job >> 8, rem = job & 255;
-            MbloDir p = mp.mbd[dir];
+            MbloDir p = P.mbd[dir];
             int row0 = (rem & 63) * 64, d0 = (rem >> 6) * 64;
             f32x4 acc1[2], acc2[2];
             #pragma unroll
@@ -737,15 +793,15 @@
             __syncthreads();
         }
     }
-    gg.sync();
+    gbar(P.bars + 2, nb);
 
     for (int job = bid; job < 512; job += nb) {
         int dir = job >> 8, rem = job & 255;
-        GDir p = mp.s2t1[dir];
-        gemm512<0, 1, 1, 1>(p.A0, nullptr, p.Wh, nullptr, p.bias, p.O0,
-                            (rem & 63) * 64, (rem >> 6) * 64, SM);
-    }
-    gg.sync();
+        GDir p = P.s2t1[dir];
+        gemm512_s((const short*)p.A0, p.Wh, p.bias, (short*)p.O0,
+                  (rem & 63) * 64, (rem >> 6) * 64, SM);
+    }
+    gbar(P.bars + 4, nb);
 
     {
         short* gAh = (short*)SM;
@@ -760,7 +816,7 @@
         int srow = tid >> 3, skl = (tid & 7) * 8;
         for (int job = bid; job < 512; job += nb) {
             int dir = job >> 8, rem = job & 255;
-            PoolDir p = mp.pld[dir];
+            PoolDir p = P.pld[dir];
             int row0 = (rem & 63) * 64, d0 = (rem >> 6) * 64;
             f32x4 acc[2];
             acc[0] = (f32x4)(0.f); acc[1] = (f32x4)(0.f);
@@ -830,7 +886,7 @@
             __syncthreads();
         }
     }
-    gg.sync();
+    gbar(P.bars + 6, nb);
 
     {
         float* sVT = (float*)SM;
@@ -840,7 +896,7 @@
         float (*red)[64] = (float(*)[64])(SM + 34816);
         for (int job = bid; job < 32; job += nb) {
             int b = job & 3, gy = (job >> 2) & 3, dir = job >> 4;
-            Gate2Dir p = mp.gtd[dir];
+            Gate2Dir p = P.gtd[dir];
             int k = tid & 255, half = tid >> 8;
             if (p.fw) {
                 #pragma unroll
@@ -926,7 +982,7 @@
             __syncthreads();
         }
     }
-    gg.sync();
+    gbar(P.bars + 8, nb);
 
     {
         float* cat = (float*)SM;
@@ -935,7 +991,7 @@
         for (int job = bid; job < 512; job += nb) {
             int dir = job >> 8, rem = job & 255;
             int bt = rem & 63, gy = rem >> 6;
-            FuseDir p = mp.fsd[dir];
+            FuseDir p = P.fsd[dir];
             int b = bt >> 4, t = bt & 15;
             size_t xrow = ((size_t)b * 1024 + t) * 256;
             if (tid < 256) {
@@ -965,7 +1021,7 @@
                 float fus = fmaxf(s1, 0.f);
                 float Gf = 1.f / (1.f + __expf(-s2));
                 float u = Gf * fus + (1.f - Gf) * cat[gc];
-                mp.out[((size_t)(b * 16 + t)) * 512 + (size_t)dir * 256 + gc] = u;
+                P.out[((size_t)(b * 16 + t)) * 512 + (size_t)dir * 256 + gc] = u;
             }
             __syncthreads();
         }
@@ -984,39 +1040,44 @@
     short* hH  = (short*)alloc(2 * 1048576 * 2);
     short* t1  = (short*)alloc(2 * 1048576 * 2);
     short* wtH = (short*)alloc(10 * 65536 * 2);
-    short* wtL = (short*)alloc(10 * 65536 * 2);
-    short* xh  = (short*)alloc(1048576 * 2);
-    short* xl  = (short*)alloc(1048576 * 2);
     float* v   = (float*)alloc(2 * 16384 * 4);
     float* E0  = (float*)alloc(2 * 1024 * 4);
-
-    SrcPack sp;
-    const int src_idx[5] = {0, 2, 3, 5, 7};
-    for (int p = 0; p < 2; p++)
-        for (int i = 0; i < 5; i++)
-            sp.s[p * 5 + i] = (const float*)d_in[1 + p * 16 + src_idx[i]];
-
-    GDir fc[2], s2t1[2];
+    unsigned* bars = (unsigned*)alloc(256);
+
+    FcPrepP fp;
+    fp.X = x;
+    const int wsrc_idx[4] = {2, 3, 5, 7};
+    for (int p = 0; p < 2; p++) {
+        int bi = 1 + p * 16;
+        fp.W0[p]  = (const float*)d_in[bi + 0];
+        fp.fcb[p] = (const float*)d_in[bi + 1];
+        fp.inH[p] = inH + (size_t)p * 1048576;
+        for (int wi = 0; wi < 4; wi++) {
+            fp.wsrc[p * 4 + wi] = (const float*)d_in[bi + wsrc_idx[wi]];
+            fp.wdst[p * 4 + wi] = wtH + (size_t)(p * 5 + 1 + wi) * 65536;
+        }
+    }
+
     MbloDir mbd[2];
+    GDir s2t1[2];
+    S2TDir std_[2];
     PoolDir pld[2];
     Gate2Dir gtd[2];
     FuseDir fsd[2];
     for (int p = 0; p < 2; p++) {
         int bi = 1 + p * 16;
-        const float* fcb   = (const float*)d_in[bi + 1];
         const float* mb    = (const float*)d_in[bi + 4];
         const float* s2tb1 = (const float*)d_in[bi + 6];
         const float* s2tb  = (const float*)d_in[bi + 8];
         size_t po = (size_t)p * 1048576;
-        const short* W0h = wtH + (size_t)(p * 5 + 0) * 65536, *W0l = wtL + (size_t)(p * 5 + 0) * 65536;
         const short* W1h = wtH + (size_t)(p * 5 + 1) * 65536;
         const short* W2h = wtH + (size_t)(p * 5 + 2) * 65536;
         const short* W3h = wtH + (size_t)(p * 5 + 3) * 65536;
         const short* W4h = wtH + (size_t)(p * 5 + 4) * 65536;
 
-        fc[p]   = { xh, xl, W0h, W0l, fcb, inH + po };
         mbd[p]  = { inH + po, W1h, W2h, mb, hH + po, (p == 0) };
         s2t1[p] = { hH + po, nullptr, W3h, nullptr, s2tb1, t1 + po };
+        std_[p] = { hH + po, W3h, s2tb1, W4h, s2tb, v + p * 16384 };
         pld[p]  = { t1 + po, W4h, s2tb, hH + po, v + p * 16384 };
         gtd[p]  = { v + p * 16384,
                     (const float*)d_in[bi + 2], (const float*)d_in[bi + 3], mb,
@@ -1027,46 +1088,38 @@
                     (const float*)d_in[bi + 14], (const float*)d_in[bi + 15] };
     }
 
-    static int coopGrid = -2;
-    if (coopGrid == -2) {
+    static int persGrid = -2;
+    if (persGrid == -2) {
         int perCU = 0;
-        hipError_t e1 = hipOccupancyMaxActiveBlocksPerMultiprocessor(&perCU, mega_k, 512, 0);
-        if (e1 == hipSuccess && perCU > 0) {
+        if (hipOccupancyMaxActiveBlocksPerMultiprocessor(&perCU, pers_k, 512, 0)
+                == hipSuccess && perCU > 0) {
             hipDeviceProp_t prop;
             int dev = 0;
             hipGetDevice(&dev);
-            if (hipGetDeviceProperties(&prop, dev) == hipSuccess && prop.cooperativeLaunch) {
-                long g = (long)perCU * prop.multiProcessorCount;
-                coopGrid = (int)(g > 512 ? 512 : g);
-            } else coopGrid = -1;
-        } else coopGrid = -1;
-    }
-
-    bool done = false;
-    if (coopGrid > 0) {
-        MegaP mp;
-        mp.sp = sp; mp.X = x;
-        mp.wtH = wtH; mp.wtL = wtL; mp.xh = xh; mp.xl = xl;
+            if (hipGetDeviceProperties(&prop, dev) == hipSuccess) {
+                long cap = (long)perCU * prop.multiProcessorCount;
+                persGrid = (int)(cap < 512 ? cap : 512);
+            } else persGrid = -1;
+        } else persGrid = -1;
+    }
+
+    if (persGrid > 0) {
+        hipMemsetAsync((void*)bars, 0, 64, stream);
+        PersP P;
+        P.X = x;
         for (int p = 0; p < 2; p++) {
-            mp.fc[p] = fc[p]; mp.s2t1[p] = s2t1[p];
-            mp.mbd[p] = mbd[p]; mp.pld[p] = pld[p];
-            mp.gtd[p] = gtd[p]; mp.fsd[p] = fsd[p];
-        }
-        mp.out = (float*)d_out;
-        void* kargs[] = { (void*)&mp };
-        if (hipLaunchCooperativeKernel((void*)mega_k, dim3(coopGrid), dim3(512),
-                                       kargs, 0, stream) == hipSuccess)
-            done = true;
-        else
-            coopGrid = -1;
-    }
-
-    if (!done) {
-        prep_k<<<dim3(16, 14), 256, 0, stream>>>(sp, x, wtH, wtL, xh, xl);
-        gemm_k<2, 1, 1, 0><<<dim3(64, 4, 2), 256, 0, stream>>>(fc[0], fc[1]);
+            P.W0[p] = fp.W0[p]; P.fcb[p] = fp.fcb[p]; P.inH[p] = fp.inH[p];
+            P.mbd[p] = mbd[p]; P.s2t1[p] = s2t1[p]; P.pld[p] = pld[p];
+            P.gtd[p] = gtd[p]; P.fsd[p] = fsd[p];
+        }
+        for (int i = 0; i < 8; i++) { P.wsrc[i] = fp.wsrc[i]; P.wdst[i] = fp.wdst[i]; }
+        P.out = (float*)d_out;
+        P.bars = bars;
+        pers_k<<<dim3(persGrid), 512, 0, stream>>>(P);
+    } else {
+        fcprep_k<<<dim3(640), 256, 0, stream>>>(fp);
         mblo_k<<<dim3(128, 4, 2), 512, 0, stream>>>(mbd[0], mbd[1]);
-        gemm_k<0, 1, 1, 1><<<dim3(64, 4, 2), 256, 0, stream>>>(s2t1[0], s2t1[1]);
-        s2t_pool_k<<<dim3(64, 4, 2), 256, 0, stream>>>(pld[0], pld[1]);
+        s2t_fused_k<<<dim3(64, 4, 2), 512, 0, stream>>>(std_[0], std_[1]);
         attn2gate_k<<<dim3(4, 4, 2), 512, 0, stream>>>(gtd[0], gtd[1]);
         fusion_k<<<dim3(64, 4, 2), 256, 0, stream>>>(fsd[0], fsd[1], (float*)d_out);
     }
```

After: 209.5 us. No clear change (-0.1%).
